# Optimization experiments

Hardware: AMD Instinct MI355X
Metric: run time of the kernel (lower is better)

## Reference

```python
import jax, jax.numpy as jnp
import numpy as np
from functools import partial

B, T, I, H = 64, 1024, 256, 256


def _lstm_dir(x_tbi, w_ih, w_hh, b_ih, b_hh, reverse):
    """Coupled-gate LSTM over time. x_tbi: [T,B,I]. Returns hs [T,B,H], (hT, cT).

    Gates = x@W_ih^T + b_ih + h@W_hh^T + b_hh, split into (in, cell, out);
    forget = 1 - in (coupled input/forget gates).
    """
    Bn = x_tbi.shape[1]
    Hn = w_hh.shape[1]
    # Precompute input contribution for all timesteps in one big GEMM.
    gx = jnp.einsum('tbi,gi->tbg', x_tbi, w_ih) + (b_ih + b_hh)  # [T,B,3H]

    def step(carry, g):
        h, c = carry
        gates = g + h @ w_hh.T  # [B,3H]
        ig, cg, og = jnp.split(gates, 3, axis=1)
        ig = jax.nn.sigmoid(ig)
        fg = 1.0 - ig
        cg = jnp.tanh(cg)
        og = jax.nn.sigmoid(og)
        c = fg * c + ig * cg
        h = og * jnp.tanh(c)
        return (h, c), h

    h0 = jnp.zeros((Bn, Hn), dtype=x_tbi.dtype)
    c0 = jnp.zeros((Bn, Hn), dtype=x_tbi.dtype)
    # lax.scan(reverse=True) runs backward in time but stacks outputs in
    # original time order, matching ReverseLSTMLayer's reverse(outputs).
    (hT, cT), hs = jax.lax.scan(step, (h0, c0), gx, reverse=reverse)
    return hs, hT, cT


def setup_inputs() -> dict:
    key = jax.random.key(0)
    ks = jax.random.split(key, 9)
    s = 0.05  # small init scale for numerical sanity
    return {
        'X': jax.random.normal(ks[0], (B, T, I), dtype=jnp.float32),
        'wih_f': jax.random.normal(ks[1], (3 * H, I), dtype=jnp.float32) * s,
        'whh_f': jax.random.normal(ks[2], (3 * H, H), dtype=jnp.float32) * s,
        'bih_f': jax.random.normal(ks[3], (3 * H,), dtype=jnp.float32) * s,
        'bhh_f': jax.random.normal(ks[4], (3 * H,), dtype=jnp.float32) * s,
        'wih_b': jax.random.normal(ks[5], (3 * H, I), dtype=jnp.float32) * s,
        'whh_b': jax.random.normal(ks[6], (3 * H, H), dtype=jnp.float32) * s,
        'bih_b': jax.random.normal(ks[7], (3 * H,), dtype=jnp.float32) * s,
        'bhh_b': jax.random.normal(ks[8], (3 * H,), dtype=jnp.float32) * s,
    }


def reference(X, wih_f, whh_f, bih_f, bhh_f, wih_b, whh_b, bih_b, bhh_b):
    x_tbi = jnp.transpose(X, (1, 0, 2))  # [T,B,I]
    hs_f, hTf, cTf = _lstm_dir(x_tbi, wih_f, whh_f, bih_f, bhh_f, reverse=False)
    hs_b, hTb, cTb = _lstm_dir(x_tbi, wih_b, whh_b, bih_b, bhh_b, reverse=True)
    out = jnp.concatenate([hs_f, hs_b], axis=-1)  # [T,B,2H]
    hn = jnp.concatenate([hTf, hTb], axis=1)[None]  # [1,B,2H]
    cn = jnp.concatenate([cTf, cTb], axis=1)[None]
    return out, hn, cn
```

## Files before the change

kernel.cpp:

```cpp
#include <hip/hip_runtime.h>
#include <cstdint>
#include <cstddef>

#define TT 1024
#define NB 64
#define HD 256
#define NG 768

typedef short bhalf8 __attribute__((ext_vector_type(8)));
typedef float f32x4  __attribute__((ext_vector_type(4)));

#define LOG2E  1.4426950408889634f
#define LOG2E2 2.8853900817779268f

__device__ __forceinline__ float bf2f(unsigned short s) {
  return __uint_as_float(((unsigned)s) << 16);
}
__device__ __forceinline__ unsigned cvt_pk_bf16(float lo, float hi) {
  unsigned r;
  asm("v_cvt_pk_bf16_f32 %0, %1, %2" : "=v"(r) : "v"(lo), "v"(hi));
  return r;
}
__device__ __forceinline__ float clamp24(float x) {
  return __builtin_amdgcn_fmed3f(x, -24.0f, 24.0f);
}
__device__ __forceinline__ void inv4(float d0, float d1, float d2, float d3,
                                     float& i0, float& i1, float& i2, float& i3) {
  float p2 = d0 * d1;
  float p3 = p2 * d2;
  float p4 = p3 * d3;
  float r  = __builtin_amdgcn_rcpf(p4);
  i3 = r * p3;
  float r3 = r * d3;
  i2 = r3 * p2;
  float r2 = r3 * d2;
  i1 = r2 * d0;
  i0 = r2 * d1;
}

#define GX_SLICE ((size_t)TT * NG * 16)

__attribute__((amdgpu_flat_work_group_size(1024, 1024)))
__attribute__((amdgpu_waves_per_eu(4, 4)))
__global__ void gx_kernel(const float* __restrict__ X,
                          const float* __restrict__ wih_f, const float* __restrict__ bih_f,
                          const float* __restrict__ bhh_f,
                          const float* __restrict__ wih_b, const float* __restrict__ bih_b,
                          const float* __restrict__ bhh_b,
                          unsigned short* __restrict__ gx) {
  const int tid = threadIdx.x;
  const int n0  = blockIdx.x * 64;
  const int t0  = blockIdx.y * 16;

  __shared__ unsigned short Al[2][64][264];

  const int lane = tid & 63, w = tid >> 6, quad = lane >> 4, l15 = lane & 15;
  const int sl = w & 3;
  const int jt = w >> 2;
  const int g  = n0 + jt * 16 + l15;
  const float wsc = (n0 >= 256 && n0 < 512) ? LOG2E2 : LOG2E;

  bhalf8 wreg[2][8];
#pragma unroll
  for (int dir = 0; dir < 2; ++dir) {
    const float* wih = dir ? wih_b : wih_f;
#pragma unroll
    for (int kt = 0; kt < 8; ++kt) {
      const float* wp = wih + (size_t)g * HD + kt * 32 + quad * 8;
      float4 v0 = *(const float4*)wp;
      float4 v1 = *(const float4*)(wp + 4);
      union { bhalf8 v; uint4 u; } pk;
      pk.u.x = cvt_pk_bf16(v0.x * wsc, v0.y * wsc);
      pk.u.y = cvt_pk_bf16(v0.z * wsc, v0.w * wsc);
      pk.u.z = cvt_pk_bf16(v1.x * wsc, v1.y * wsc);
      pk.u.w = cvt_pk_bf16(v1.z * wsc, v1.w * wsc);
      wreg[dir][kt] = pk.v;
    }
  }
  const float bias_f = (bih_f[g] + bhh_f[g]) * wsc;
  const float bias_b = (bih_b[g] + bhh_b[g]) * wsc;

#define STAGE_X(ttv, buf)                                                     \
  {                                                                           \
    const int t = t0 + (ttv);                                                 \
    _Pragma("unroll")                                                         \
    for (int i = 0; i < 4; ++i) {                                             \
      int f4  = tid + i * 1024;                                               \
      int row = f4 >> 6;                                                      \
      int kk  = (f4 & 63) * 4;                                                \
      float4 xv = *(const float4*)(X + ((size_t)row * TT + t) * HD + kk);     \
      uint2 p;                                                                \
      p.x = cvt_pk_bf16(xv.x, xv.y);                                          \
      p.y = cvt_pk_bf16(xv.z, xv.w);                                          \
      *(uint2*)&Al[buf][row][kk] = p;                                         \
    }                                                                         \
  }

  STAGE_X(0, 0);

  for (int tt = 0; tt < 16; ++tt) {
    const int buf = tt & 1;
    __syncthreads();
    if (tt < 15) STAGE_X(tt + 1, buf ^ 1);

    f32x4 acc0 = {0.f, 0.f, 0.f, 0.f};
    f32x4 acc1 = {0.f, 0.f, 0.f, 0.f};
#pragma unroll
    for (int kt = 0; kt < 8; ++kt) {
      bhalf8 a = *(const bhalf8*)&Al[buf][16 * sl + l15][kt * 32 + quad * 8];
      acc0 = __builtin_amdgcn_mfma_f32_16x16x32_bf16(a, wreg[0][kt], acc0, 0, 0, 0);
      acc1 = __builtin_amdgcn_mfma_f32_16x16x32_bf16(a, wreg[1][kt], acc1, 0, 0, 0);
    }

    const int t = t0 + tt;
    {
      unsigned short* gs = gx + sl * GX_SLICE + (size_t)t * NG * 16 + g * 16 + quad * 4;
      uint2 p;
      p.x = cvt_pk_bf16(acc0[0] + bias_f, acc0[1] + bias_f);
      p.y = cvt_pk_bf16(acc0[2] + bias_f, acc0[3] + bias_f);
      *(uint2*)gs = p;
      unsigned short* gs1 = gs + 4 * GX_SLICE;
      uint2 q;
      q.x = cvt_pk_bf16(acc1[0] + bias_b, acc1[1] + bias_b);
      q.y = cvt_pk_bf16(acc1[2] + bias_b, acc1[3] + bias_b);
      *(uint2*)gs1 = q;
    }
  }
#undef STAGE_X
}

__attribute__((amdgpu_flat_work_group_size(1024, 1024)))
__attribute__((amdgpu_waves_per_eu(4, 4)))
__global__ void rec_kernel(const float* __restrict__ whh_f,
                           const float* __restrict__ whh_b,
                           const unsigned short* __restrict__ gx,
                           float* __restrict__ out) {
  const int tid  = threadIdx.x;
  const int lane = tid & 63, w = tid >> 6, quad = lane >> 4, l15 = lane & 15;
  const int blk = blockIdx.x;
  const int dir = blk >> 2;
  const int b0  = (blk & 3) * 16;
  const float* whh = dir ? whh_b : whh_f;
  const unsigned short* gxd = gx + (size_t)dir * 4 * GX_SLICE + (size_t)(blk & 3) * GX_SLICE;
  float* hn = out + (size_t)TT * NB * 512;
  float* cn = hn + (size_t)NB * 512;

  __shared__ uint4 wlds[16][8][64];
  __shared__ uint4 hk[2][8][64];

  bhalf8 wreg[2][8];
#pragma unroll
  for (int p = 0; p < 3; ++p) {
    int n = p * 256 + 16 * w + l15;
    const float wscp = (p == 1) ? LOG2E2 : LOG2E;
#pragma unroll
    for (int kt = 0; kt < 8; ++kt) {
      const float* wp = whh + (size_t)n * HD + kt * 32 + quad * 8;
      float4 v0 = *(const float4*)wp;
      float4 v1 = *(const float4*)(wp + 4);
      union { bhalf8 v; uint4 u; } pk;
      pk.u.x = cvt_pk_bf16(v0.x * wscp, v0.y * wscp);
      pk.u.y = cvt_pk_bf16(v0.z * wscp, v0.w * wscp);
      pk.u.z = cvt_pk_bf16(v1.x * wscp, v1.y * wscp);
      pk.u.w = cvt_pk_bf16(v1.z * wscp, v1.w * wscp);
      if (p < 2) wreg[p][kt] = pk.v;
      else       wlds[w][kt][lane] = pk.u;
    }
  }

  if (tid < 512) {
    uint4 z; z.x = z.y = z.z = z.w = 0;
    ((uint4*)hk[0])[tid] = z;
  }

  float cstate[4];
#pragma unroll
  for (int r = 0; r < 4; ++r) cstate[r] = 0.0f;

  int goff[3];
#pragma unroll
  for (int p = 0; p < 3; ++p) {
    int g = p * 256 + 16 * w + l15;
    goff[p] = g * 16 + quad * 4;
  }

  __syncthreads();

  const unsigned short* gptr = gxd + (size_t)(dir ? (TT - 1) : 0) * NG * 16;
  const ptrdiff_t gstep = dir ? -(ptrdiff_t)((size_t)NG * 16) : (ptrdiff_t)((size_t)NG * 16);

  float* orow = out + ((size_t)(dir ? (TT - 1) : 0) * NB + b0 + quad * 4) * 512
                + dir * 256 + 16 * w + l15;
  const ptrdiff_t ostep = dir ? -(ptrdiff_t)(NB * 512) : (ptrdiff_t)(NB * 512);

  ushort4 gxv[3];
#pragma unroll
  for (int p = 0; p < 3; ++p) gxv[p] = *(const ushort4*)(gptr + goff[p]);

#pragma unroll 2
  for (int s = 0; s < TT; ++s) {
    const int pb = s & 1;

    f32x4 acc[3];
#pragma unroll
    for (int p = 0; p < 3; ++p) {
      acc[p][0] = bf2f(gxv[p].x); acc[p][1] = bf2f(gxv[p].y);
      acc[p][2] = bf2f(gxv[p].z); acc[p][3] = bf2f(gxv[p].w);
    }
    gptr += gstep;
#pragma unroll
    for (int p = 0; p < 3; ++p) gxv[p] = *(const ushort4*)(gptr + goff[p]);

#pragma unroll
    for (int kt = 0; kt < 8; ++kt) {
      bhalf8 a = __builtin_bit_cast(bhalf8, hk[pb][kt][lane]);
      acc[0] = __builtin_amdgcn_mfma_f32_16x16x32_bf16(a, wreg[0][kt], acc[0], 0, 0, 0);
      acc[1] = __builtin_amdgcn_mfma_f32_16x16x32_bf16(a, wreg[1][kt], acc[1], 0, 0, 0);
      acc[2] = __builtin_amdgcn_mfma_f32_16x16x32_bf16(
          a, __builtin_bit_cast(bhalf8, wlds[w][kt][lane]), acc[2], 0, 0, 0);
    }

    unsigned short* hnext = (unsigned short*)hk[pb ^ 1][w >> 1];
    float ei[4], ec[4], eo[4];
#pragma unroll
    for (int r = 0; r < 4; ++r) {
      ei[r] = __builtin_amdgcn_exp2f(clamp24(-acc[0][r]));
      ec[r] = __builtin_amdgcn_exp2f(clamp24( acc[1][r]));
      eo[r] = __builtin_amdgcn_exp2f(clamp24(-acc[2][r]));
    }
    float ig[4], tc[4], og[4];
    inv4(1.f + ei[0], 1.f + ei[1], 1.f + ei[2], 1.f + ei[3],
         ig[0], ig[1], ig[2], ig[3]);
    inv4(1.f + ec[0], 1.f + ec[1], 1.f + ec[2], 1.f + ec[3],
         tc[0], tc[1], tc[2], tc[3]);
    inv4(1.f + eo[0], 1.f + eo[1], 1.f + eo[2], 1.f + eo[3],
         og[0], og[1], og[2], og[3]);
    float cvv[4], et[4];
#pragma unroll
    for (int r = 0; r < 4; ++r) {
      float cg = __builtin_fmaf(-2.f, tc[r], 1.f);
      float cp = cstate[r];
      float cv = __builtin_fmaf(ig[r], cg - cp, cp);
      cstate[r] = cv;
      cvv[r] = cv;
      et[r] = __builtin_amdgcn_exp2f(cv * LOG2E2);
    }
    float it4[4];
    inv4(1.f + et[0], 1.f + et[1], 1.f + et[2], 1.f + et[3],
         it4[0], it4[1], it4[2], it4[3]);
    float hv[4];
#pragma unroll
    for (int r = 0; r < 4; ++r)
      hv[r] = og[r] * __builtin_fmaf(-2.f, it4[r], 1.f);

    unsigned short* hbj = hnext
        + (size_t)(((((w & 1) * 2 + (l15 >> 3)) * 16) + quad * 4) * 8) + (l15 & 7);
    unsigned u01 = cvt_pk_bf16(hv[0], hv[1]);
    unsigned u23 = cvt_pk_bf16(hv[2], hv[3]);
    hbj[0]  = (unsigned short)u01;
    hbj[8]  = (unsigned short)(u01 >> 16);
    hbj[16] = (unsigned short)u23;
    hbj[24] = (unsigned short)(u23 >> 16);

#pragma unroll
    for (int r = 0; r < 4; ++r) {
      orow[(size_t)r * 512 + 0] = hv[r];
      if (s == TT - 1) {
        int brow = b0 + quad * 4 + r;
        int col  = 16 * w + l15;
        hn[(size_t)brow * 512 + dir * 256 + col] = hv[r];
        cn[(size_t)brow * 512 + dir * 256 + col] = cvv[r];
      }
    }
    orow += ostep;
    __syncthreads();
  }
}

extern "C" void kernel_launch(void* const* d_in, const int* in_sizes, int n_in,
                              void* d_out, int out_size, void* d_ws, size_t ws_size,
                              hipStream_t stream) {
  const float* X     = (const float*)d_in[0];
  const float* wih_f = (const float*)d_in[1];
  const float* whh_f = (const float*)d_in[2];
  const float* bih_f = (const float*)d_in[3];
  const float* bhh_f = (const float*)d_in[4];
  const float* wih_b = (const float*)d_in[5];
  const float* whh_b = (const float*)d_in[6];
  const float* bih_b = (const float*)d_in[7];
  const float* bhh_b = (const float*)d_in[8];
  float* out = (float*)d_out;
  unsigned short* gxbuf = (unsigned short*)d_ws;

  dim3 g1(NG / 64, TT / 16);
  gx_kernel<<<g1, 1024, 0, stream>>>(X, wih_f, bih_f, bhh_f, wih_b, bih_b, bhh_b, gxbuf);
  rec_kernel<<<8, 1024, 0, stream>>>(whh_f, whh_b, gxbuf, out);
}
```

Baseline: 1.898 ms.

## Split LSTM recurrence across paired blocks with global-memory hidden-state exchange

```diff
diff --git a/kernel.cpp b/kernel.cpp
--- a/kernel.cpp
+++ b/kernel.cpp
@@ -40,6 +40,9 @@
 
 #define GX_SLICE ((size_t)TT * NG * 16)
 
+__device__ uint2    hxch[2][16][512];
+__device__ unsigned rec_flags[16];
+
 __attribute__((amdgpu_flat_work_group_size(1024, 1024)))
 __attribute__((amdgpu_waves_per_eu(4, 4)))
 __global__ void gx_kernel(const float* __restrict__ X,
@@ -49,8 +52,13 @@
                           const float* __restrict__ bhh_b,
                           unsigned short* __restrict__ gx) {
   const int tid = threadIdx.x;
-  const int n0  = blockIdx.x * 64;
-  const int t0  = blockIdx.y * 16;
+  const int bid  = blockIdx.x;
+  const int xcd  = bid & 7;
+  const int i    = bid >> 3;
+  const int n0   = (i % 12) * 64;
+  const int t0   = (xcd + 8 * (i / 12)) * 16;
+
+  if (bid == 0 && tid < 16) rec_flags[tid] = 0;
 
   __shared__ unsigned short Al[2][64][264];
 
@@ -84,8 +92,8 @@
   {                                                                           \
     const int t = t0 + (ttv);                                                 \
     _Pragma("unroll")                                                         \
-    for (int i = 0; i < 4; ++i) {                                             \
-      int f4  = tid + i * 1024;                                               \
+    for (int ii = 0; ii < 4; ++ii) {                                          \
+      int f4  = tid + ii * 1024;                                              \
       int row = f4 >> 6;                                                      \
       int kk  = (f4 & 63) * 4;                                                \
       float4 xv = *(const float4*)(X + ((size_t)row * TT + t) * HD + kk);     \
@@ -129,29 +137,32 @@
 #undef STAGE_X
 }
 
-__attribute__((amdgpu_flat_work_group_size(1024, 1024)))
-__attribute__((amdgpu_waves_per_eu(4, 4)))
+__attribute__((amdgpu_flat_work_group_size(512, 512)))
+__attribute__((amdgpu_waves_per_eu(2, 2)))
 __global__ void rec_kernel(const float* __restrict__ whh_f,
                            const float* __restrict__ whh_b,
                            const unsigned short* __restrict__ gx,
                            float* __restrict__ out) {
   const int tid  = threadIdx.x;
   const int lane = tid & 63, w = tid >> 6, quad = lane >> 4, l15 = lane & 15;
-  const int blk = blockIdx.x;
-  const int dir = blk >> 2;
-  const int b0  = (blk & 3) * 16;
+  const int bid  = blockIdx.x;
+  const int half = bid >> 3;
+  const int r3   = bid & 7;
+  const int dir  = r3 >> 2;
+  const int b0   = (r3 & 3) * 16;
+  const int pbid = bid ^ 8;
   const float* whh = dir ? whh_b : whh_f;
-  const unsigned short* gxd = gx + (size_t)dir * 4 * GX_SLICE + (size_t)(blk & 3) * GX_SLICE;
+  const unsigned short* gxd = gx + (size_t)dir * 4 * GX_SLICE + (size_t)(r3 & 3) * GX_SLICE;
   float* hn = out + (size_t)TT * NB * 512;
   float* cn = hn + (size_t)NB * 512;
 
-  __shared__ uint4 wlds[16][8][64];
+  __shared__ uint4 wlds[8][8][64];
   __shared__ uint4 hk[2][8][64];
 
   bhalf8 wreg[2][8];
 #pragma unroll
   for (int p = 0; p < 3; ++p) {
-    int n = p * 256 + 16 * w + l15;
+    int n = p * 256 + half * 128 + 16 * w + l15;
     const float wscp = (p == 1) ? LOG2E2 : LOG2E;
 #pragma unroll
     for (int kt = 0; kt < 8; ++kt) {
@@ -168,7 +179,7 @@
     }
   }
 
-  if (tid < 512) {
+  {
     uint4 z; z.x = z.y = z.z = z.w = 0;
     ((uint4*)hk[0])[tid] = z;
   }
@@ -180,9 +191,13 @@
   int goff[3];
 #pragma unroll
   for (int p = 0; p < 3; ++p) {
-    int g = p * 256 + 16 * w + l15;
+    int g = p * 256 + half * 128 + 16 * w + l15;
     goff[p] = g * 16 + quad * 4;
   }
+
+  const int ktb_own  = half * 4 + (w >> 1);
+  const int ktb_par  = (1 - half) * 4 + (w >> 1);
+  const int chunk_base = (((w & 1) * 2 + (l15 >> 3)) * 16 + quad * 4) * 8 + (l15 & 7);
 
   __syncthreads();
 
@@ -190,7 +205,7 @@
   const ptrdiff_t gstep = dir ? -(ptrdiff_t)((size_t)NG * 16) : (ptrdiff_t)((size_t)NG * 16);
 
   float* orow = out + ((size_t)(dir ? (TT - 1) : 0) * NB + b0 + quad * 4) * 512
-                + dir * 256 + 16 * w + l15;
+                + dir * 256 + half * 128 + 16 * w + l15;
   const ptrdiff_t ostep = dir ? -(ptrdiff_t)(NB * 512) : (ptrdiff_t)(NB * 512);
 
   ushort4 gxv[3];
@@ -220,7 +235,6 @@
           a, __builtin_bit_cast(bhalf8, wlds[w][kt][lane]), acc[2], 0, 0, 0);
     }
 
-    unsigned short* hnext = (unsigned short*)hk[pb ^ 1][w >> 1];
     float ei[4], ec[4], eo[4];
 #pragma unroll
     for (int r = 0; r < 4; ++r) {
@@ -253,8 +267,7 @@
     for (int r = 0; r < 4; ++r)
       hv[r] = og[r] * __builtin_fmaf(-2.f, it4[r], 1.f);
 
-    unsigned short* hbj = hnext
-        + (size_t)(((((w & 1) * 2 + (l15 >> 3)) * 16) + quad * 4) * 8) + (l15 & 7);
+    unsigned short* hbj = (unsigned short*)hk[pb ^ 1][ktb_own] + chunk_base;
     unsigned u01 = cvt_pk_bf16(hv[0], hv[1]);
     unsigned u23 = cvt_pk_bf16(hv[2], hv[3]);
     hbj[0]  = (unsigned short)u01;
@@ -263,17 +276,39 @@
     hbj[24] = (unsigned short)(u23 >> 16);
 
 #pragma unroll
-    for (int r = 0; r < 4; ++r) {
-      orow[(size_t)r * 512 + 0] = hv[r];
-      if (s == TT - 1) {
+    for (int r = 0; r < 4; ++r) orow[(size_t)r * 512] = hv[r];
+    orow += ostep;
+
+    if (s < TT - 1) {
+      uint2 px; px.x = u01; px.y = u23;
+      hxch[(s + 1) & 1][bid][tid] = px;
+      __syncthreads();
+      if (tid == 0) {
+        __builtin_amdgcn_fence(__ATOMIC_RELEASE, "agent");
+        __hip_atomic_store(&rec_flags[bid], (unsigned)(s + 1),
+                           __ATOMIC_RELAXED, __HIP_MEMORY_SCOPE_AGENT);
+      }
+      while (__hip_atomic_load(&rec_flags[pbid], __ATOMIC_RELAXED,
+                               __HIP_MEMORY_SCOPE_AGENT) < (unsigned)(s + 1)) {
+        __builtin_amdgcn_s_sleep(1);
+      }
+      __builtin_amdgcn_fence(__ATOMIC_ACQUIRE, "agent");
+      uint2 qx = hxch[(s + 1) & 1][pbid][tid];
+      unsigned short* pbj = (unsigned short*)hk[pb ^ 1][ktb_par] + chunk_base;
+      pbj[0]  = (unsigned short)qx.x;
+      pbj[8]  = (unsigned short)(qx.x >> 16);
+      pbj[16] = (unsigned short)qx.y;
+      pbj[24] = (unsigned short)(qx.y >> 16);
+      __syncthreads();
+    } else {
+#pragma unroll
+      for (int r = 0; r < 4; ++r) {
         int brow = b0 + quad * 4 + r;
-        int col  = 16 * w + l15;
+        int col  = half * 128 + 16 * w + l15;
         hn[(size_t)brow * 512 + dir * 256 + col] = hv[r];
         cn[(size_t)brow * 512 + dir * 256 + col] = cvv[r];
       }
     }
-    orow += ostep;
-    __syncthreads();
   }
 }
 
@@ -292,7 +327,6 @@
   float* out = (float*)d_out;
   unsigned short* gxbuf = (unsigned short*)d_ws;
 
-  dim3 g1(NG / 64, TT / 16);
-  gx_kernel<<<g1, 1024, 0, stream>>>(X, wih_f, bih_f, bhh_f, wih_b, bih_b, bhh_b, gxbuf);
-  rec_kernel<<<8, 1024, 0, stream>>>(whh_f, whh_b, gxbuf, out);
-}
+  gx_kernel<<<768, 1024, 0, stream>>>(X, wih_f, bih_f, bhh_f, wih_b, bih_b, bhh_b, gxbuf);
+  rec_kernel<<<16, 512, 0, stream>>>(whh_f, whh_b, gxbuf, out);
+}
```

Measured after the change: 3.872 ms. 104% more time.
